# Optimization experiments

Hardware: AMD Instinct MI355X
Metric: run time of the kernel (lower is better)

## Reference

```python
import jax, jax.numpy as jnp
from jax import lax
import numpy as np

B, C, D, H, W = 2, 2, 128, 256, 256
N_PAIRS = 32
N_ITERS = 10
SMOOTH = 1e-5


def setup_inputs() -> dict:
    key = jax.random.key(0)
    k1, k2 = jax.random.split(key)
    logits = jax.random.normal(k1, (B, C, D, H, W), dtype=jnp.float32)
    labels = jax.random.randint(k2, (B, 1, D, H, W), 0, 2).astype(jnp.int32)
    # Replicate the torch module's endpoint sampling (nonzero + randint) with numpy,
    # since it is non-differentiable index bookkeeping, not part of the loss math.
    lab_np = np.asarray(labels)
    rng = np.random.default_rng(0)
    ea = np.zeros((B, N_PAIRS, 3), dtype=np.int32)
    eb = np.zeros((B, N_PAIRS, 3), dtype=np.int32)
    for b in range(B):
        coords = np.argwhere(lab_np[b, 0] > 0)  # (n_fg, 3)
        n_fg = coords.shape[0]
        ia = rng.integers(0, n_fg, size=N_PAIRS)
        ib = rng.integers(0, n_fg, size=N_PAIRS)
        same = ia == ib
        ib[same] = (ib[same] + 1) % n_fg
        ea[b] = coords[ia]
        eb[b] = coords[ib]
    return {
        "logits": logits,
        "labels": labels,
        "endpoints_a": jnp.asarray(ea),
        "endpoints_b": jnp.asarray(eb),
    }


def _avg_pool3d(x):
    # 3x3x3 box filter, stride 1, zero padding, count_include_pad=True (torch default)
    s = lax.reduce_window(x, 0.0, lax.add, (3, 3, 3), (1, 1, 1), "SAME")
    return s / 27.0


def _pair_connectivity(prob, ea, eb):
    # prob: (D,H,W); ea/eb: (n_pairs, 3) int source/target voxel coords
    heat = jnp.zeros_like(prob).at[ea[:, 0], ea[:, 1], ea[:, 2]].set(1.0)

    def step(h, _):
        h = _avg_pool3d(h) * prob
        hmax = h.max()
        h = jnp.where(hmax > 0, h / (hmax + SMOOTH), h)
        return h, None

    heat, _ = lax.scan(step, heat, None, length=N_ITERS)
    scores = heat[eb[:, 0], eb[:, 1], eb[:, 2]]
    return 1.0 - scores.mean()


def reference(logits, labels, endpoints_a, endpoints_b):
    # labels only determined endpoint sampling (done in setup_inputs); loss math uses logits.
    fg_prob = jax.nn.softmax(logits, axis=1)[:, 1]  # (B, D, H, W)
    per_batch = jax.vmap(_pair_connectivity)(fg_prob, endpoints_a, endpoints_b)
    return per_batch.mean()
```

## Files before the change

### kernel.cpp

```cpp
#include <hip/hip_runtime.h>
#include <cstddef>

#define BZ   2
#define DV   128
#define HV   256
#define WV   256
#define NP   32
#define NBOX (BZ*NP)
#define NIT  10
#define RAD  10
#define BOX  21
#define BOXP 24
#define UBOXSZ (BOX*BOX*BOXP)
#define HWV  65536
#define DHW  ((size_t)DV*HWV)
#define SMOOTH 1e-5f

__global__ void __launch_bounds__(512)
evolve_kernel(const float* __restrict__ logits,
              const int* __restrict__ ea,
              float* __restrict__ u,
              float* __restrict__ g9part,
              int* __restrict__ dupflag)
{
    __shared__ float A[UBOXSZ];
    __shared__ float sred[8];
    __shared__ int sflag;

    const int box = blockIdx.x;
    const int b = box >> 5;
    const int t = threadIdx.x;

    const int sd = ea[box*3+0], sh = ea[box*3+1], sw = ea[box*3+2];

    if (t == 0) {
        int dup = 0;
        for (int q = b*NP; q < box; ++q)
            if (ea[q*3] == sd && ea[q*3+1] == sh && ea[q*3+2] == sw) { dup = 1; break; }
        sflag = dup;
        dupflag[box] = dup;
        if (dup) g9part[box] = 0.f;
    }
    __syncthreads();
    if (sflag) return;

    for (int i = t; i < UBOXSZ; i += 512) A[i] = 0.f;
    __syncthreads();
    if (t == 0) A[(RAD*BOX + RAD)*BOXP + RAD] = 1.0f;

    float p[BOX];
    const int hh = (t < 441) ? t / BOX : 0;
    const int ww = (t < 441) ? t % BOX : 0;
    #pragma unroll
    for (int d = 0; d < BOX; ++d) p[d] = 0.f;
    if (t < 441) {
        const int gh = sh - RAD + hh;
        const int gw = sw - RAD + ww;
        if (gh >= 0 && gh < HV && gw >= 0 && gw < WV) {
            const float* lg = logits + (size_t)b * 2 * DHW;
            #pragma unroll
            for (int d = 0; d < BOX; ++d) {
                int gd = sd - RAD + d;
                if (gd >= 0 && gd < DV) {
                    size_t off = (size_t)gd * HWV + (size_t)gh * WV + gw;
                    float l0 = lg[off], l1 = lg[off + DHW];
                    p[d] = 1.f / (1.f + __expf(l0 - l1));
                }
            }
        }
    }
    __syncthreads();

    const int dA = t / BOX;
    const int hA = t % BOX;

    for (int k = 0; k < NIT; ++k) {
        if (t < 441) {
            float* base = &A[(dA*BOX + hA)*BOXP];
            float r[BOX];
            #pragma unroll
            for (int i = 0; i < 5; ++i) {
                float4 q = ((float4*)base)[i];
                r[4*i] = q.x; r[4*i+1] = q.y; r[4*i+2] = q.z; r[4*i+3] = q.w;
            }
            r[20] = base[20];
            float s[BOX];
            #pragma unroll
            for (int w = 0; w < BOX; ++w) {
                float a = (w > 0)  ? r[w-1] : 0.f;
                float c = (w < 20) ? r[w+1] : 0.f;
                s[w] = a + r[w] + c;
            }
            #pragma unroll
            for (int i = 0; i < 5; ++i)
                ((float4*)base)[i] = make_float4(s[4*i], s[4*i+1], s[4*i+2], s[4*i+3]);
            base[20] = s[20];
        }
        __syncthreads();
        if (t < 441) {
            const int d = dA, w = hA;
            float c[BOX];
            #pragma unroll
            for (int h = 0; h < BOX; ++h) c[h] = A[(d*BOX + h)*BOXP + w];
            #pragma unroll
            for (int h = 0; h < BOX; ++h) {
                float a = (h > 0)  ? c[h-1] : 0.f;
                float e = (h < 20) ? c[h+1] : 0.f;
                A[(d*BOX + h)*BOXP + w] = a + c[h] + e;
            }
        }
        __syncthreads();
        float mymax = 0.f;
        if (t < 441) {
            float c[BOX];
            #pragma unroll
            for (int d = 0; d < BOX; ++d) c[d] = A[(d*BOX + hh)*BOXP + ww];
            #pragma unroll
            for (int d = 0; d < BOX; ++d) {
                float a = (d > 0)  ? c[d-1] : 0.f;
                float e = (d < 20) ? c[d+1] : 0.f;
                float v = (a + c[d] + e) * p[d] * (1.f/27.f);
                A[(d*BOX + hh)*BOXP + ww] = v;
                if (k == NIT-2) mymax = fmaxf(mymax, v);
            }
        }
        if (k == NIT-2) {
            #pragma unroll
            for (int o = 32; o > 0; o >>= 1)
                mymax = fmaxf(mymax, __shfl_down(mymax, o));
            if ((t & 63) == 0) sred[t >> 6] = mymax;
            __syncthreads();
            if (t == 0) {
                float m = sred[0];
                for (int i = 1; i < 8; ++i) m = fmaxf(m, sred[i]);
                g9part[box] = m;
            }
        }
        __syncthreads();
    }

    float4* dst = (float4*)(u + (size_t)box * UBOXSZ);
    const float4* src = (const float4*)A;
    for (int i = t; i < UBOXSZ/4; i += 512) dst[i] = src[i];
}

__global__ void __launch_bounds__(256)
maxsum_kernel(const int* __restrict__ ea,
              const float* __restrict__ u,
              const int* __restrict__ dupflag,
              float* __restrict__ gNpart)
{
    const int box = blockIdx.x;
    const int b = box >> 5;
    const int t = threadIdx.x;

    if (dupflag[box]) { if (t == 0) gNpart[box] = 0.f; return; }

    __shared__ int list[NP];
    __shared__ int lseed[NP][3];
    __shared__ int nlist, myseed[3];
    __shared__ float sred[4];
    if (t == 0) {
        int n = 0;
        int sd = ea[box*3], sh = ea[box*3+1], sw = ea[box*3+2];
        myseed[0] = sd; myseed[1] = sh; myseed[2] = sw;
        for (int q = b*NP; q < (b+1)*NP; ++q) {
            if (q == box || dupflag[q]) continue;
            int qd = ea[q*3], qh = ea[q*3+1], qw = ea[q*3+2];
            if (abs(qd - sd) <= 2*RAD && abs(qh - sh) <= 2*RAD && abs(qw - sw) <= 2*RAD) {
                list[n] = q;
                lseed[n][0] = qd; lseed[n][1] = qh; lseed[n][2] = qw;
                ++n;
            }
        }
        nlist = n;
    }
    __syncthreads();

    const int sd = myseed[0], sh = myseed[1], sw = myseed[2];
    const int nl = nlist;
    float m = 0.f;
    for (int i = t; i < BOX*BOX*BOX; i += 256) {
        int d = i / (BOX*BOX), r = i % (BOX*BOX);
        int h = r / BOX, w = r % BOX;
        float v = u[(size_t)box * UBOXSZ + (d*BOX + h)*BOXP + w];
        int gd = sd - RAD + d, gh = sh - RAD + h, gw = sw - RAD + w;
        for (int j = 0; j < nl; ++j) {
            int ld = gd - lseed[j][0] + RAD;
            int lh = gh - lseed[j][1] + RAD;
            int lw = gw - lseed[j][2] + RAD;
            if (ld >= 0 && ld < BOX && lh >= 0 && lh < BOX && lw >= 0 && lw < BOX)
                v += u[(size_t)list[j] * UBOXSZ + (ld*BOX + lh)*BOXP + lw];
        }
        m = fmaxf(m, v);
    }
    #pragma unroll
    for (int o = 32; o > 0; o >>= 1) m = fmaxf(m, __shfl_down(m, o));
    if ((t & 63) == 0) sred[t >> 6] = m;
    __syncthreads();
    if (t == 0)
        gNpart[box] = fmaxf(fmaxf(sred[0], sred[1]), fmaxf(sred[2], sred[3]));
}

__global__ void final_kernel(const int* __restrict__ ea,
                             const int* __restrict__ eb,
                             const float* __restrict__ u,
                             const int* __restrict__ dupflag,
                             const float* __restrict__ gNpart,
                             const float* __restrict__ g9part,
                             float* __restrict__ out)
{
    const int t = threadIdx.x;
    const int b = t >> 5;
    float gN = 0.f, g9 = 0.f;
    for (int q = b*NP; q < (b+1)*NP; ++q) {
        gN = fmaxf(gN, gNpart[q]);
        g9 = fmaxf(g9, g9part[q]);
    }
    const float tden = gN + SMOOTH * g9;

    const int d = eb[t*3], h = eb[t*3+1], w = eb[t*3+2];
    float v = 0.f;
    for (int q = b*NP; q < (b+1)*NP; ++q) {
        if (dupflag[q]) continue;
        int ld = d - ea[q*3]   + RAD;
        int lh = h - ea[q*3+1] + RAD;
        int lw = w - ea[q*3+2] + RAD;
        if (ld >= 0 && ld < BOX && lh >= 0 && lh < BOX && lw >= 0 && lw < BOX)
            v += u[(size_t)q * UBOXSZ + (ld*BOX + lh)*BOXP + lw];
    }
    float score = (tden > 0.f) ? v / tden : 0.f;
    #pragma unroll
    for (int o = 32; o > 0; o >>= 1) score += __shfl_down(score, o);
    if (t == 0) out[0] = 1.f - score / (float)(BZ * NP);
}

extern "C" void kernel_launch(void* const* d_in, const int* in_sizes, int n_in,
                              void* d_out, int out_size, void* d_ws, size_t ws_size,
                              hipStream_t stream) {
    const float* logits = (const float*)d_in[0];
    const int* ea = (const int*)d_in[2];
    const int* eb = (const int*)d_in[3];
    float* out = (float*)d_out;

    float* u      = (float*)d_ws;
    float* g9part = u + (size_t)NBOX * UBOXSZ;
    float* gNpart = g9part + NBOX;
    int*   dflag  = (int*)(gNpart + NBOX);

    evolve_kernel<<<NBOX, 512, 0, stream>>>(logits, ea, u, g9part, dflag);
    maxsum_kernel<<<NBOX, 256, 0, stream>>>(ea, u, dflag, gNpart);
    final_kernel<<<1, 64, 0, stream>>>(ea, eb, u, dflag, gNpart, g9part, out);
}
```

Measured before the change: 260.8 us.

## Compact LDS box layout, stream stencil passes, compute local max in evolve kernel

```diff
diff --git a/kernel.cpp b/kernel.cpp
--- a/kernel.cpp
+++ b/kernel.cpp
@@ -10,8 +10,8 @@
 #define NIT  10
 #define RAD  10
 #define BOX  21
-#define BOXP 24
-#define UBOXSZ (BOX*BOX*BOXP)
+#define BOX2 (BOX*BOX)
+#define BOX3 (BOX*BOX*BOX)
 #define HWV  65536
 #define DHW  ((size_t)DV*HWV)
 #define SMOOTH 1e-5f
@@ -21,10 +21,11 @@
               const int* __restrict__ ea,
               float* __restrict__ u,
               float* __restrict__ g9part,
+              float* __restrict__ gNpart,
               int* __restrict__ dupflag)
 {
-    __shared__ float A[UBOXSZ];
-    __shared__ float sred[8];
+    __shared__ float A[BOX3];
+    __shared__ float sred9[8], sredN[8];
     __shared__ int sflag;
 
     const int box = blockIdx.x;
@@ -39,21 +40,20 @@
             if (ea[q*3] == sd && ea[q*3+1] == sh && ea[q*3+2] == sw) { dup = 1; break; }
         sflag = dup;
         dupflag[box] = dup;
-        if (dup) g9part[box] = 0.f;
+        if (dup) { g9part[box] = 0.f; gNpart[box] = 0.f; }
     }
     __syncthreads();
     if (sflag) return;
 
-    for (int i = t; i < UBOXSZ; i += 512) A[i] = 0.f;
-    __syncthreads();
-    if (t == 0) A[(RAD*BOX + RAD)*BOXP + RAD] = 1.0f;
+    for (int i = t; i < BOX3; i += 512) A[i] = 0.f;
+    __syncthreads();
+    if (t == 0) A[RAD*BOX2 + RAD*BOX + RAD] = 1.0f;
 
     float p[BOX];
-    const int hh = (t < 441) ? t / BOX : 0;
-    const int ww = (t < 441) ? t % BOX : 0;
     #pragma unroll
     for (int d = 0; d < BOX; ++d) p[d] = 0.f;
-    if (t < 441) {
+    if (t < BOX2) {
+        const int hh = t / BOX, ww = t % BOX;
         const int gh = sh - RAD + hh;
         const int gw = sw - RAD + ww;
         if (gh >= 0 && gh < HV && gw >= 0 && gw < WV) {
@@ -64,84 +64,70 @@
                 if (gd >= 0 && gd < DV) {
                     size_t off = (size_t)gd * HWV + (size_t)gh * WV + gw;
                     float l0 = lg[off], l1 = lg[off + DHW];
-                    p[d] = 1.f / (1.f + __expf(l0 - l1));
+                    p[d] = (1.f/27.f) / (1.f + __expf(l0 - l1));
                 }
             }
         }
     }
     __syncthreads();
 
-    const int dA = t / BOX;
-    const int hA = t % BOX;
+    float max9 = 0.f, maxN = 0.f;
 
     for (int k = 0; k < NIT; ++k) {
-        if (t < 441) {
-            float* base = &A[(dA*BOX + hA)*BOXP];
-            float r[BOX];
-            #pragma unroll
-            for (int i = 0; i < 5; ++i) {
-                float4 q = ((float4*)base)[i];
-                r[4*i] = q.x; r[4*i+1] = q.y; r[4*i+2] = q.z; r[4*i+3] = q.w;
-            }
-            r[20] = base[20];
-            float s[BOX];
+        if (t < BOX2) {
+            const int base = t * BOX;
+            float prev = 0.f, cur = A[base], nxt;
             #pragma unroll
             for (int w = 0; w < BOX; ++w) {
-                float a = (w > 0)  ? r[w-1] : 0.f;
-                float c = (w < 20) ? r[w+1] : 0.f;
-                s[w] = a + r[w] + c;
-            }
-            #pragma unroll
-            for (int i = 0; i < 5; ++i)
-                ((float4*)base)[i] = make_float4(s[4*i], s[4*i+1], s[4*i+2], s[4*i+3]);
-            base[20] = s[20];
+                nxt = (w < BOX-1) ? A[base + w + 1] : 0.f;
+                A[base + w] = prev + cur + nxt;
+                prev = cur; cur = nxt;
+            }
         }
         __syncthreads();
-        if (t < 441) {
-            const int d = dA, w = hA;
-            float c[BOX];
-            #pragma unroll
-            for (int h = 0; h < BOX; ++h) c[h] = A[(d*BOX + h)*BOXP + w];
+        if (t < BOX2) {
+            const int d = t / BOX, w = t % BOX;
+            const int base = d * BOX2 + w;
+            float prev = 0.f, cur = A[base], nxt;
             #pragma unroll
             for (int h = 0; h < BOX; ++h) {
-                float a = (h > 0)  ? c[h-1] : 0.f;
-                float e = (h < 20) ? c[h+1] : 0.f;
-                A[(d*BOX + h)*BOXP + w] = a + c[h] + e;
+                nxt = (h < BOX-1) ? A[base + (h+1)*BOX] : 0.f;
+                A[base + h*BOX] = prev + cur + nxt;
+                prev = cur; cur = nxt;
             }
         }
         __syncthreads();
-        float mymax = 0.f;
-        if (t < 441) {
-            float c[BOX];
-            #pragma unroll
-            for (int d = 0; d < BOX; ++d) c[d] = A[(d*BOX + hh)*BOXP + ww];
+        if (t < BOX2) {
+            float prev = 0.f, cur = A[t], nxt;
             #pragma unroll
             for (int d = 0; d < BOX; ++d) {
-                float a = (d > 0)  ? c[d-1] : 0.f;
-                float e = (d < 20) ? c[d+1] : 0.f;
-                float v = (a + c[d] + e) * p[d] * (1.f/27.f);
-                A[(d*BOX + hh)*BOXP + ww] = v;
-                if (k == NIT-2) mymax = fmaxf(mymax, v);
-            }
-        }
-        if (k == NIT-2) {
-            #pragma unroll
-            for (int o = 32; o > 0; o >>= 1)
-                mymax = fmaxf(mymax, __shfl_down(mymax, o));
-            if ((t & 63) == 0) sred[t >> 6] = mymax;
-            __syncthreads();
-            if (t == 0) {
-                float m = sred[0];
-                for (int i = 1; i < 8; ++i) m = fmaxf(m, sred[i]);
-                g9part[box] = m;
+                nxt = (d < BOX-1) ? A[(d+1)*BOX2 + t] : 0.f;
+                float v = (prev + cur + nxt) * p[d];
+                A[d*BOX2 + t] = v;
+                prev = cur; cur = nxt;
+                if (k == NIT-2) max9 = fmaxf(max9, v);
+                if (k == NIT-1) maxN = fmaxf(maxN, v);
             }
         }
         __syncthreads();
     }
 
-    float4* dst = (float4*)(u + (size_t)box * UBOXSZ);
-    const float4* src = (const float4*)A;
-    for (int i = t; i < UBOXSZ/4; i += 512) dst[i] = src[i];
+    #pragma unroll
+    for (int o = 32; o > 0; o >>= 1) {
+        max9 = fmaxf(max9, __shfl_down(max9, o));
+        maxN = fmaxf(maxN, __shfl_down(maxN, o));
+    }
+    if ((t & 63) == 0) { sred9[t >> 6] = max9; sredN[t >> 6] = maxN; }
+    __syncthreads();
+    if (t == 0) {
+        float m9 = sred9[0], mN = sredN[0];
+        #pragma unroll
+        for (int i = 1; i < 8; ++i) { m9 = fmaxf(m9, sred9[i]); mN = fmaxf(mN, sredN[i]); }
+        g9part[box] = m9;
+        gNpart[box] = mN;
+    }
+
+    for (int i = t; i < BOX3; i += 512) u[(size_t)box * BOX3 + i] = A[i];
 }
 
 __global__ void __launch_bounds__(256)
@@ -154,43 +140,47 @@
     const int b = box >> 5;
     const int t = threadIdx.x;
 
-    if (dupflag[box]) { if (t == 0) gNpart[box] = 0.f; return; }
-
     __shared__ int list[NP];
     __shared__ int lseed[NP][3];
     __shared__ int nlist, myseed[3];
     __shared__ float sred[4];
+
     if (t == 0) {
         int n = 0;
         int sd = ea[box*3], sh = ea[box*3+1], sw = ea[box*3+2];
         myseed[0] = sd; myseed[1] = sh; myseed[2] = sw;
-        for (int q = b*NP; q < (b+1)*NP; ++q) {
-            if (q == box || dupflag[q]) continue;
-            int qd = ea[q*3], qh = ea[q*3+1], qw = ea[q*3+2];
-            if (abs(qd - sd) <= 2*RAD && abs(qh - sh) <= 2*RAD && abs(qw - sw) <= 2*RAD) {
-                list[n] = q;
-                lseed[n][0] = qd; lseed[n][1] = qh; lseed[n][2] = qw;
-                ++n;
+        if (!dupflag[box]) {
+            for (int q = b*NP; q < (b+1)*NP; ++q) {
+                if (q == box || dupflag[q]) continue;
+                int qd = ea[q*3], qh = ea[q*3+1], qw = ea[q*3+2];
+                if (abs(qd - sd) <= 2*RAD && abs(qh - sh) <= 2*RAD &&
+                    abs(qw - sw) <= 2*RAD) {
+                    list[n] = q;
+                    lseed[n][0] = qd; lseed[n][1] = qh; lseed[n][2] = qw;
+                    ++n;
+                }
             }
         }
         nlist = n;
     }
     __syncthreads();
 
+    const int nl = nlist;
+    if (nl == 0) return;
+
     const int sd = myseed[0], sh = myseed[1], sw = myseed[2];
-    const int nl = nlist;
     float m = 0.f;
-    for (int i = t; i < BOX*BOX*BOX; i += 256) {
-        int d = i / (BOX*BOX), r = i % (BOX*BOX);
+    for (int i = t; i < BOX3; i += 256) {
+        int d = i / BOX2, r = i % BOX2;
         int h = r / BOX, w = r % BOX;
-        float v = u[(size_t)box * UBOXSZ + (d*BOX + h)*BOXP + w];
+        float v = u[(size_t)box * BOX3 + i];
         int gd = sd - RAD + d, gh = sh - RAD + h, gw = sw - RAD + w;
         for (int j = 0; j < nl; ++j) {
             int ld = gd - lseed[j][0] + RAD;
             int lh = gh - lseed[j][1] + RAD;
             int lw = gw - lseed[j][2] + RAD;
             if (ld >= 0 && ld < BOX && lh >= 0 && lh < BOX && lw >= 0 && lw < BOX)
-                v += u[(size_t)list[j] * UBOXSZ + (ld*BOX + lh)*BOXP + lw];
+                v += u[(size_t)list[j] * BOX3 + (ld*BOX + lh)*BOX + lw];
         }
         m = fmaxf(m, v);
     }
@@ -227,7 +217,7 @@
         int lh = h - ea[q*3+1] + RAD;
         int lw = w - ea[q*3+2] + RAD;
         if (ld >= 0 && ld < BOX && lh >= 0 && lh < BOX && lw >= 0 && lw < BOX)
-            v += u[(size_t)q * UBOXSZ + (ld*BOX + lh)*BOXP + lw];
+            v += u[(size_t)q * BOX3 + (ld*BOX + lh)*BOX + lw];
     }
     float score = (tden > 0.f) ? v / tden : 0.f;
     #pragma unroll
@@ -244,11 +234,11 @@
     float* out = (float*)d_out;
 
     float* u      = (float*)d_ws;
-    float* g9part = u + (size_t)NBOX * UBOXSZ;
+    float* g9part = u + (size_t)NBOX * BOX3;
     float* gNpart = g9part + NBOX;
     int*   dflag  = (int*)(gNpart + NBOX);
 
-    evolve_kernel<<<NBOX, 512, 0, stream>>>(logits, ea, u, g9part, dflag);
+    evolve_kernel<<<NBOX, 512, 0, stream>>>(logits, ea, u, g9part, gNpart, dflag);
     maxsum_kernel<<<NBOX, 256, 0, stream>>>(ea, u, dflag, gNpart);
     final_kernel<<<1, 64, 0, stream>>>(ea, eb, u, dflag, gNpart, g9part, out);
 }
```

Result: faster. 253.7 us (-2.7%).
